# Kernel optimization log

Hardware: AMD Instinct MI355X
Metric: run time of the kernel (lower is better)

The kernel has to match this reference:

```python
import jax, jax.numpy as jnp
import numpy as np

# Uniform 3-level taxonomy: 128 roots, branching 16 then 16.
N0, B1, B2 = 128, 16, 16
N1, N2 = N0 * B1, N0 * B1 * B2          # 2048, 32768
TOTAL = N0 + N1 + N2                    # 34944
BATCH = 1024
W = (1.0, 1.0, 1.0)                     # level_weights
NEG = -100000000.0                      # fill value used by the torch module


def _ce(logits, tgt):
    # per-sample cross entropy, reduction='none': logits [B,C], tgt [B] -> [B]
    return -jnp.take_along_axis(jax.nn.log_softmax(logits, axis=-1), tgt[:, None], axis=1)[:, 0]


def setup_inputs() -> dict:
    key = jax.random.key(0)
    k1, k2, k3, k4 = jax.random.split(key, 4)
    outputs = jax.random.normal(k1, (BATCH, TOTAL), dtype=jnp.float32)
    # hierarchically consistent labels (relative-within-level ids, as labelmap expects)
    r0 = jax.random.randint(k2, (BATCH,), 0, N0, dtype=jnp.int32)
    r1 = jax.random.randint(k3, (BATCH,), 0, B1, dtype=jnp.int32)
    r2 = jax.random.randint(k4, (BATCH,), 0, B2, dtype=jnp.int32)
    lab1 = r0 * B1 + r1
    lab2 = lab1 * B2 + r2
    level_labels = jnp.stack([r0, lab1, lab2], axis=1)  # [B, 3] int32
    return {"outputs": outputs, "level_labels": level_labels}


def reference(outputs, level_labels):
    lab0, lab1, lab2 = level_labels[:, 0], level_labels[:, 1], level_labels[:, 2]
    r1 = lab1 - lab0 * B1   # new_level_labels[1]: label relative to true parent's children
    r2 = lab2 - lab1 * B2   # new_level_labels[2]

    out0 = outputs[:, :N0]                 # [B, N0]
    out1 = outputs[:, N0:N0 + N1]          # [B, N1]
    out2 = outputs[:, N0 + N1:]            # [B, N2]

    # ---- level 0: possible children == all roots, so masked CE == full CE
    loss0 = _ce(out0, lab0)
    pred0 = jnp.argmax(out0, axis=1).astype(jnp.int32)          # predicted root (relative)
    found0 = pred0 != lab0                                      # found_incorrect after level 0

    # ---- level 1
    g1_true = jnp.take_along_axis(out1.reshape(BATCH, N0, B1), lab0[:, None, None], axis=1)[:, 0, :]
    loss1 = jnp.where(found0, _ce(out1, lab1), _ce(g1_true, r1))
    g1_pred = jnp.take_along_axis(out1.reshape(BATCH, N0, B1), pred0[:, None, None], axis=1)[:, 0, :]
    pred1_in = jnp.argmax(g1_pred, axis=1).astype(jnp.int32)    # argmax within predicted parent's children
    pred1 = pred0 * B1 + pred1_in                               # predicted level-1 class (relative)
    found1 = found0 | (pred1_in != r1)

    # ---- level 2
    g2_true = jnp.take_along_axis(out2.reshape(BATCH, N1, B2), lab1[:, None, None], axis=1)[:, 0, :]
    loss2 = jnp.where(found1, _ce(out2, lab2), _ce(g2_true, r2))

    # ---- outputs_new: level-0 slice fully copied; levels 1/2 only children of the predicted path
    mask1 = (jnp.arange(N1, dtype=jnp.int32) // B1)[None, :] == pred0[:, None]
    mask2 = (jnp.arange(N2, dtype=jnp.int32) // B2)[None, :] == pred1[:, None]
    outputs_new = jnp.concatenate(
        [out0, jnp.where(mask1, out1, NEG), jnp.where(mask2, out2, NEG)], axis=1)

    # torch accumulates size-1 tensors; torch.mean of the final [1] tensor == total sum
    loss = jnp.sum(W[0] * loss0 + W[1] * loss1 + W[2] * loss2)
    return outputs_new, loss
```

## Files before the change

### kernel.cpp

```cpp
#include <hip/hip_runtime.h>
#include <math.h>

#define N0v 128
#define B1v 16
#define B2v 16
#define N1v 2048
#define N2v 32768
#define TOTALv 34944
#define BATCHv 1024
#define NEGV -100000000.0f

typedef __attribute__((ext_vector_type(4))) float f32x4;

__global__ __launch_bounds__(1024) void row_kernel(
    const float* __restrict__ outs, const int* __restrict__ labels,
    float* __restrict__ out, float* __restrict__ partials)
{
    const int b   = blockIdx.x;
    const int tid = threadIdx.x;
    const int wid = tid >> 6, lane = tid & 63;
    const float* rowp = outs + (size_t)b * TOTALv;
    float*       orow = out  + (size_t)b * TOTALv;
    const f32x4* rv4 = reinterpret_cast<const f32x4*>(rowp);
    f32x4*       ov4 = reinterpret_cast<f32x4*>(orow);
    const f32x4  neg4 = {NEGV, NEGV, NEGV, NEGV};

    __shared__ float s_wmax[2]; __shared__ int s_wmi[2];
    __shared__ float s_r[16][3];
    __shared__ float s_f[1];
    __shared__ int   s_i[2];
    __shared__ float s_g[2];

    const int lab0 = labels[b * 3 + 0];
    const int lab1 = labels[b * 3 + 1];
    const int lab2 = labels[b * 3 + 2];

    float v0 = -INFINITY;
    if (tid < N0v) v0 = rowp[tid];
    f32x4 a = {0.f, 0.f, 0.f, 0.f};
    if (tid < 512) a = rv4[32 + tid];
    const f32x4* b2 = rv4 + 544;
    f32x4*       o2 = ov4 + 544;
    const f32x4 x0 = b2[tid];
    const f32x4 x1 = b2[tid + 1024];
    const f32x4 x2 = b2[tid + 2048];
    const f32x4 x3 = b2[tid + 3072];
    const f32x4 x4 = b2[tid + 4096];
    const f32x4 x5 = b2[tid + 5120];
    const f32x4 x6 = b2[tid + 6144];
    const f32x4 x7 = b2[tid + 7168];
    __builtin_amdgcn_sched_barrier(0);

    float mv = v0; int mi = tid;
    #pragma unroll
    for (int off = 32; off; off >>= 1) {
        float ov = __shfl_down(mv, off);
        int   oi = __shfl_down(mi, off);
        if (ov > mv || (ov == mv && oi < mi)) { mv = ov; mi = oi; }
    }
    if (tid < N0v && lane == 0) { s_wmax[wid] = mv; s_wmi[wid] = mi; }
    __syncthreads();
    if (tid == 0) {
        float m0 = s_wmax[0]; int i0 = s_wmi[0];
        if (s_wmax[1] > m0 || (s_wmax[1] == m0 && s_wmi[1] < i0)) { m0 = s_wmax[1]; i0 = s_wmi[1]; }
        s_f[0] = m0; s_i[0] = i0;
    }
    __syncthreads();
    const float max0  = s_f[0];
    const int   pred0 = s_i[0];

    if (tid < 16) {
        float gp = rowp[N0v + pred0 * B1v + tid]; int gi = tid;
        #pragma unroll
        for (int off = 8; off; off >>= 1) {
            float ogp = __shfl_xor(gp, off, 16);
            int   ogi = __shfl_xor(gi, off, 16);
            if (ogp > gp || (ogp == gp && ogi < gi)) { gp = ogp; gi = ogi; }
        }
        if (tid == 0) s_i[1] = gi;
    } else if (tid < 32) {
        float eg = __expf(rowp[N0v + lab0 * B1v + (tid - 16)]);
        #pragma unroll
        for (int off = 8; off; off >>= 1) eg += __shfl_xor(eg, off, 16);
        if (tid == 16) s_g[0] = eg;
    } else if (tid < 48) {
        float eg = __expf(rowp[N0v + N1v + lab1 * B2v + (tid - 32)]);
        #pragma unroll
        for (int off = 8; off; off >>= 1) eg += __shfl_xor(eg, off, 16);
        if (tid == 32) s_g[1] = eg;
    }
    __syncthreads();
    const int pred1_in = s_i[1];
    const int pred1    = pred0 * B1v + pred1_in;

    float s1 = 0.f;
    if (tid < 512) {
        s1 = __expf(a.x) + __expf(a.y) + __expf(a.z) + __expf(a.w);
        __builtin_nontemporal_store((tid >> 2) == pred0 ? a : neg4, &ov4[32 + tid]);
        if (tid < N0v) __builtin_nontemporal_store(v0, &orow[tid]);
    }

    float s2 = 0.f;
    s2 += __expf(x0.x)+__expf(x0.y)+__expf(x0.z)+__expf(x0.w);
    __builtin_nontemporal_store(((tid       ) >> 2) == pred1 ? x0 : neg4, &o2[tid]);
    s2 += __expf(x1.x)+__expf(x1.y)+__expf(x1.z)+__expf(x1.w);
    __builtin_nontemporal_store(((tid + 1024) >> 2) == pred1 ? x1 : neg4, &o2[tid + 1024]);
    s2 += __expf(x2.x)+__expf(x2.y)+__expf(x2.z)+__expf(x2.w);
    __builtin_nontemporal_store(((tid + 2048) >> 2) == pred1 ? x2 : neg4, &o2[tid + 2048]);
    s2 += __expf(x3.x)+__expf(x3.y)+__expf(x3.z)+__expf(x3.w);
    __builtin_nontemporal_store(((tid + 3072) >> 2) == pred1 ? x3 : neg4, &o2[tid + 3072]);
    s2 += __expf(x4.x)+__expf(x4.y)+__expf(x4.z)+__expf(x4.w);
    __builtin_nontemporal_store(((tid + 4096) >> 2) == pred1 ? x4 : neg4, &o2[tid + 4096]);
    s2 += __expf(x5.x)+__expf(x5.y)+__expf(x5.z)+__expf(x5.w);
    __builtin_nontemporal_store(((tid + 5120) >> 2) == pred1 ? x5 : neg4, &o2[tid + 5120]);
    s2 += __expf(x6.x)+__expf(x6.y)+__expf(x6.z)+__expf(x6.w);
    __builtin_nontemporal_store(((tid + 6144) >> 2) == pred1 ? x6 : neg4, &o2[tid + 6144]);
    s2 += __expf(x7.x)+__expf(x7.y)+__expf(x7.z)+__expf(x7.w);
    __builtin_nontemporal_store(((tid + 7168) >> 2) == pred1 ? x7 : neg4, &o2[tid + 7168]);

    float r0 = (tid < N0v) ? __expf(v0 - max0) : 0.f;
    #pragma unroll
    for (int off = 32; off; off >>= 1) {
        r0 += __shfl_down(r0, off);
        s1 += __shfl_down(s1, off);
        s2 += __shfl_down(s2, off);
    }
    if (lane == 0) { s_r[wid][0] = r0; s_r[wid][1] = s1; s_r[wid][2] = s2; }
    __syncthreads();
    if (tid == 0) {
        float S0 = 0.f, S1 = 0.f, S2 = 0.f;
        #pragma unroll
        for (int w = 0; w < 16; ++w) { S0 += s_r[w][0]; S1 += s_r[w][1]; S2 += s_r[w][2]; }
        const float Sg1 = s_g[0], Sg2 = s_g[1];
        const int r1 = lab1 - lab0 * B1v;
        const bool found0 = (pred0 != lab0);
        const bool found1 = found0 || (pred1_in != r1);
        const float t0 = rowp[lab0];
        const float t1 = rowp[N0v + lab1];
        const float t2 = rowp[N0v + N1v + lab2];
        const float loss0 = __logf(S0) + max0 - t0;
        const float loss1 = (found0 ? __logf(S1) : __logf(Sg1)) - t1;
        const float loss2 = (found1 ? __logf(S2) : __logf(Sg2)) - t2;
        partials[b] = loss0 + loss1 + loss2;
    }
}

__global__ __launch_bounds__(256) void loss_reduce(
    const float* __restrict__ partials, float* __restrict__ out_loss)
{
    __shared__ float sh[4];
    const int tid = threadIdx.x;
    float s = 0.f;
    for (int i = tid; i < BATCHv; i += 256) s += partials[i];
    #pragma unroll
    for (int off = 32; off; off >>= 1) s += __shfl_down(s, off);
    if ((tid & 63) == 0) sh[tid >> 6] = s;
    __syncthreads();
    if (tid == 0) *out_loss = sh[0] + sh[1] + sh[2] + sh[3];
}

extern "C" void kernel_launch(void* const* d_in, const int* in_sizes, int n_in,
                              void* d_out, int out_size, void* d_ws, size_t ws_size,
                              hipStream_t stream) {
    const float* outs   = (const float*)d_in[0];
    const int*   labels = (const int*)d_in[1];
    float*       out    = (float*)d_out;
    float*       part   = (float*)d_ws;

    row_kernel<<<BATCHv, 1024, 0, stream>>>(outs, labels, out, part);
    loss_reduce<<<1, 256, 0, stream>>>(part, out + (size_t)BATCHv * TOTALv);
}
```

Before: 53.46 us.

## Split each row across two 512-thread blocks and cut per-row sync barriers

Each row is now handled by two 512-thread blocks, each taking half of the level-2 slice. The level-1 group sums and argmaxes are computed once for all 128 groups from registers, so the dependent pred0 gather and its barriers go away. Stores are deferred until after a single barrier, and the level-2 log-sum is combined across the two halves in the finalize kernel. The max subtraction for level 0 is dropped, which risks overflow with unbounded inputs, and level-1 data is loaded twice per row.

```diff
diff --git a/kernel.cpp b/kernel.cpp
--- a/kernel.cpp
+++ b/kernel.cpp
@@ -12,151 +12,157 @@
 
 typedef __attribute__((ext_vector_type(4))) float f32x4;
 
-__global__ __launch_bounds__(1024) void row_kernel(
+__global__ __launch_bounds__(512, 8) void row_kernel(
     const float* __restrict__ outs, const int* __restrict__ labels,
-    float* __restrict__ out, float* __restrict__ partials)
+    float* __restrict__ out, float* __restrict__ s2p, float* __restrict__ lb)
 {
-    const int b   = blockIdx.x;
+    const int blk = blockIdx.x;
+    const int row = blk >> 1;
+    const int j   = blk & 1;
     const int tid = threadIdx.x;
     const int wid = tid >> 6, lane = tid & 63;
-    const float* rowp = outs + (size_t)b * TOTALv;
-    float*       orow = out  + (size_t)b * TOTALv;
+    const float* rowp = outs + (size_t)row * TOTALv;
+    float*       orow = out  + (size_t)row * TOTALv;
     const f32x4* rv4 = reinterpret_cast<const f32x4*>(rowp);
     f32x4*       ov4 = reinterpret_cast<f32x4*>(orow);
     const f32x4  neg4 = {NEGV, NEGV, NEGV, NEGV};
 
+    __shared__ float sm_gsum[128];
+    __shared__ int   sm_gidx[128];
     __shared__ float s_wmax[2]; __shared__ int s_wmi[2];
-    __shared__ float s_r[16][3];
-    __shared__ float s_f[1];
+    __shared__ float s_red[8][3];
     __shared__ int   s_i[2];
-    __shared__ float s_g[2];
 
-    const int lab0 = labels[b * 3 + 0];
-    const int lab1 = labels[b * 3 + 1];
-    const int lab2 = labels[b * 3 + 2];
+    const int lab0 = labels[row * 3 + 0];
+    const int lab1 = labels[row * 3 + 1];
+    const int lab2 = labels[row * 3 + 2];
 
-    float v0 = -INFINITY;
+    float v0 = 0.f;
     if (tid < N0v) v0 = rowp[tid];
-    f32x4 a = {0.f, 0.f, 0.f, 0.f};
-    if (tid < 512) a = rv4[32 + tid];
-    const f32x4* b2 = rv4 + 544;
-    f32x4*       o2 = ov4 + 544;
-    const f32x4 x0 = b2[tid];
-    const f32x4 x1 = b2[tid + 1024];
-    const f32x4 x2 = b2[tid + 2048];
-    const f32x4 x3 = b2[tid + 3072];
-    const f32x4 x4 = b2[tid + 4096];
-    const f32x4 x5 = b2[tid + 5120];
-    const f32x4 x6 = b2[tid + 6144];
-    const f32x4 x7 = b2[tid + 7168];
+    const f32x4 a = rv4[32 + tid];
+    const f32x4* b2 = rv4 + 544 + j * 4096;
+    f32x4*       o2 = ov4 + 544 + j * 4096;
+    const f32x4 x0 = b2[tid];            const f32x4 x1 = b2[tid +  512];
+    const f32x4 x2 = b2[tid + 1024];     const f32x4 x3 = b2[tid + 1536];
+    const f32x4 x4 = b2[tid + 2048];     const f32x4 x5 = b2[tid + 2560];
+    const f32x4 x6 = b2[tid + 3072];     const f32x4 x7 = b2[tid + 3584];
+    float eg2 = 0.f;
+    if (tid < 16) eg2 = rowp[N0v + N1v + lab1 * B2v + tid];
+    float t0 = 0.f, t1 = 0.f, t2 = 0.f;
+    if (tid == 0) { t0 = rowp[lab0]; t1 = rowp[N0v + lab1]; t2 = rowp[N0v + N1v + lab2]; }
     __builtin_amdgcn_sched_barrier(0);
 
-    float mv = v0; int mi = tid;
-    #pragma unroll
-    for (int off = 32; off; off >>= 1) {
-        float ov = __shfl_down(mv, off);
-        int   oi = __shfl_down(mi, off);
-        if (ov > mv || (ov == mv && oi < mi)) { mv = ov; mi = oi; }
+    float s1 = __expf(a.x) + __expf(a.y) + __expf(a.z) + __expf(a.w);
+    float gm = a.x; int gi = 0;
+    if (a.y > gm) { gm = a.y; gi = 1; }
+    if (a.z > gm) { gm = a.z; gi = 2; }
+    if (a.w > gm) { gm = a.w; gi = 3; }
+    gi += (tid & 3) * 4;
+    float gs = s1;
+    {
+        float ov = __shfl_xor(gm, 1); int oi = __shfl_xor(gi, 1);
+        gs += __shfl_xor(gs, 1);
+        if (ov > gm || (ov == gm && oi < gi)) { gm = ov; gi = oi; }
+        ov = __shfl_xor(gm, 2); oi = __shfl_xor(gi, 2);
+        gs += __shfl_xor(gs, 2);
+        if (ov > gm || (ov == gm && oi < gi)) { gm = ov; gi = oi; }
     }
-    if (tid < N0v && lane == 0) { s_wmax[wid] = mv; s_wmi[wid] = mi; }
-    __syncthreads();
-    if (tid == 0) {
-        float m0 = s_wmax[0]; int i0 = s_wmi[0];
-        if (s_wmax[1] > m0 || (s_wmax[1] == m0 && s_wmi[1] < i0)) { m0 = s_wmax[1]; i0 = s_wmi[1]; }
-        s_f[0] = m0; s_i[0] = i0;
+    if ((tid & 3) == 0) { sm_gsum[tid >> 2] = gs; sm_gidx[tid >> 2] = gi; }
+
+    if (tid < N0v) {
+        float mv = v0; int mi = tid;
+        #pragma unroll
+        for (int off = 32; off; off >>= 1) {
+            float ov = __shfl_down(mv, off);
+            int   oi = __shfl_down(mi, off);
+            if (ov > mv || (ov == mv && oi < mi)) { mv = ov; mi = oi; }
+        }
+        if (lane == 0) { s_wmax[wid] = mv; s_wmi[wid] = mi; }
     }
-    __syncthreads();
-    const float max0  = s_f[0];
-    const int   pred0 = s_i[0];
 
     if (tid < 16) {
-        float gp = rowp[N0v + pred0 * B1v + tid]; int gi = tid;
+        eg2 = __expf(eg2);
         #pragma unroll
-        for (int off = 8; off; off >>= 1) {
-            float ogp = __shfl_xor(gp, off, 16);
-            int   ogi = __shfl_xor(gi, off, 16);
-            if (ogp > gp || (ogp == gp && ogi < gi)) { gp = ogp; gi = ogi; }
-        }
-        if (tid == 0) s_i[1] = gi;
-    } else if (tid < 32) {
-        float eg = __expf(rowp[N0v + lab0 * B1v + (tid - 16)]);
-        #pragma unroll
-        for (int off = 8; off; off >>= 1) eg += __shfl_xor(eg, off, 16);
-        if (tid == 16) s_g[0] = eg;
-    } else if (tid < 48) {
-        float eg = __expf(rowp[N0v + N1v + lab1 * B2v + (tid - 32)]);
-        #pragma unroll
-        for (int off = 8; off; off >>= 1) eg += __shfl_xor(eg, off, 16);
-        if (tid == 32) s_g[1] = eg;
-    }
-    __syncthreads();
-    const int pred1_in = s_i[1];
-    const int pred1    = pred0 * B1v + pred1_in;
-
-    float s1 = 0.f;
-    if (tid < 512) {
-        s1 = __expf(a.x) + __expf(a.y) + __expf(a.z) + __expf(a.w);
-        __builtin_nontemporal_store((tid >> 2) == pred0 ? a : neg4, &ov4[32 + tid]);
-        if (tid < N0v) __builtin_nontemporal_store(v0, &orow[tid]);
+        for (int off = 8; off; off >>= 1) eg2 += __shfl_xor(eg2, off);
     }
 
     float s2 = 0.f;
     s2 += __expf(x0.x)+__expf(x0.y)+__expf(x0.z)+__expf(x0.w);
-    __builtin_nontemporal_store(((tid       ) >> 2) == pred1 ? x0 : neg4, &o2[tid]);
     s2 += __expf(x1.x)+__expf(x1.y)+__expf(x1.z)+__expf(x1.w);
-    __builtin_nontemporal_store(((tid + 1024) >> 2) == pred1 ? x1 : neg4, &o2[tid + 1024]);
     s2 += __expf(x2.x)+__expf(x2.y)+__expf(x2.z)+__expf(x2.w);
-    __builtin_nontemporal_store(((tid + 2048) >> 2) == pred1 ? x2 : neg4, &o2[tid + 2048]);
     s2 += __expf(x3.x)+__expf(x3.y)+__expf(x3.z)+__expf(x3.w);
-    __builtin_nontemporal_store(((tid + 3072) >> 2) == pred1 ? x3 : neg4, &o2[tid + 3072]);
     s2 += __expf(x4.x)+__expf(x4.y)+__expf(x4.z)+__expf(x4.w);
-    __builtin_nontemporal_store(((tid + 4096) >> 2) == pred1 ? x4 : neg4, &o2[tid + 4096]);
     s2 += __expf(x5.x)+__expf(x5.y)+__expf(x5.z)+__expf(x5.w);
-    __builtin_nontemporal_store(((tid + 5120) >> 2) == pred1 ? x5 : neg4, &o2[tid + 5120]);
     s2 += __expf(x6.x)+__expf(x6.y)+__expf(x6.z)+__expf(x6.w);
-    __builtin_nontemporal_store(((tid + 6144) >> 2) == pred1 ? x6 : neg4, &o2[tid + 6144]);
     s2 += __expf(x7.x)+__expf(x7.y)+__expf(x7.z)+__expf(x7.w);
-    __builtin_nontemporal_store(((tid + 7168) >> 2) == pred1 ? x7 : neg4, &o2[tid + 7168]);
 
-    float r0 = (tid < N0v) ? __expf(v0 - max0) : 0.f;
+    float r0 = (tid < N0v) ? __expf(v0) : 0.f;
     #pragma unroll
     for (int off = 32; off; off >>= 1) {
         r0 += __shfl_down(r0, off);
         s1 += __shfl_down(s1, off);
         s2 += __shfl_down(s2, off);
     }
-    if (lane == 0) { s_r[wid][0] = r0; s_r[wid][1] = s1; s_r[wid][2] = s2; }
+    if (lane == 0) { s_red[wid][0] = r0; s_red[wid][1] = s1; s_red[wid][2] = s2; }
+
     __syncthreads();
+
     if (tid == 0) {
+        float m0 = s_wmax[0]; int p0 = s_wmi[0];
+        if (s_wmax[1] > m0 || (s_wmax[1] == m0 && s_wmi[1] < p0)) { m0 = s_wmax[1]; p0 = s_wmi[1]; }
+        const int p1i = sm_gidx[p0];
+        s_i[0] = p0; s_i[1] = p1i;
         float S0 = 0.f, S1 = 0.f, S2 = 0.f;
         #pragma unroll
-        for (int w = 0; w < 16; ++w) { S0 += s_r[w][0]; S1 += s_r[w][1]; S2 += s_r[w][2]; }
-        const float Sg1 = s_g[0], Sg2 = s_g[1];
-        const int r1 = lab1 - lab0 * B1v;
-        const bool found0 = (pred0 != lab0);
-        const bool found1 = found0 || (pred1_in != r1);
-        const float t0 = rowp[lab0];
-        const float t1 = rowp[N0v + lab1];
-        const float t2 = rowp[N0v + N1v + lab2];
-        const float loss0 = __logf(S0) + max0 - t0;
-        const float loss1 = (found0 ? __logf(S1) : __logf(Sg1)) - t1;
-        const float loss2 = (found1 ? __logf(S2) : __logf(Sg2)) - t2;
-        partials[b] = loss0 + loss1 + loss2;
+        for (int w = 0; w < 8; ++w) { S0 += s_red[w][0]; S1 += s_red[w][1]; S2 += s_red[w][2]; }
+        s2p[row * 2 + j] = S2;
+        if (j == 0) {
+            const float Sg1 = sm_gsum[lab0];
+            const int r1 = lab1 - lab0 * B1v;
+            const bool found0 = (p0 != lab0);
+            const bool found1 = found0 || (p1i != r1);
+            const float loss01 = (__logf(S0) - t0)
+                               + ((found0 ? __logf(S1) : __logf(Sg1)) - t1);
+            lb[row * 2 + 0] = loss01 - t2 + (found1 ? 0.f : __logf(eg2));
+            lb[row * 2 + 1] = found1 ? 1.f : 0.f;
+        }
     }
+    __syncthreads();
+    const int pred0 = s_i[0];
+    const int pred1 = pred0 * B1v + s_i[1];
+
+    if (j == 0 && tid < N0v) __builtin_nontemporal_store(v0, &orow[tid]);
+    if ((tid >> 8) == j)
+        __builtin_nontemporal_store(((tid >> 2) == pred0) ? a : neg4, &ov4[32 + tid]);
+    const int lbase = j * 4096;
+    __builtin_nontemporal_store((((lbase + tid       ) >> 2) == pred1) ? x0 : neg4, &o2[tid]);
+    __builtin_nontemporal_store((((lbase + tid +  512) >> 2) == pred1) ? x1 : neg4, &o2[tid +  512]);
+    __builtin_nontemporal_store((((lbase + tid + 1024) >> 2) == pred1) ? x2 : neg4, &o2[tid + 1024]);
+    __builtin_nontemporal_store((((lbase + tid + 1536) >> 2) == pred1) ? x3 : neg4, &o2[tid + 1536]);
+    __builtin_nontemporal_store((((lbase + tid + 2048) >> 2) == pred1) ? x4 : neg4, &o2[tid + 2048]);
+    __builtin_nontemporal_store((((lbase + tid + 2560) >> 2) == pred1) ? x5 : neg4, &o2[tid + 2560]);
+    __builtin_nontemporal_store((((lbase + tid + 3072) >> 2) == pred1) ? x6 : neg4, &o2[tid + 3072]);
+    __builtin_nontemporal_store((((lbase + tid + 3584) >> 2) == pred1) ? x7 : neg4, &o2[tid + 3584]);
 }
 
-__global__ __launch_bounds__(256) void loss_reduce(
-    const float* __restrict__ partials, float* __restrict__ out_loss)
+__global__ __launch_bounds__(1024) void finalize_kernel(
+    const float* __restrict__ s2p, const float* __restrict__ lb,
+    float* __restrict__ out_loss)
 {
-    __shared__ float sh[4];
-    const int tid = threadIdx.x;
-    float s = 0.f;
-    for (int i = tid; i < BATCHv; i += 256) s += partials[i];
+    const int r = threadIdx.x;
+    const float S2 = s2p[r * 2] + s2p[r * 2 + 1];
+    float loss = lb[r * 2] + lb[r * 2 + 1] * __logf(S2);
     #pragma unroll
-    for (int off = 32; off; off >>= 1) s += __shfl_down(s, off);
-    if ((tid & 63) == 0) sh[tid >> 6] = s;
+    for (int off = 32; off; off >>= 1) loss += __shfl_down(loss, off);
+    __shared__ float sh[16];
+    if ((r & 63) == 0) sh[r >> 6] = loss;
     __syncthreads();
-    if (tid == 0) *out_loss = sh[0] + sh[1] + sh[2] + sh[3];
+    if (r == 0) {
+        float t = 0.f;
+        #pragma unroll
+        for (int w = 0; w < 16; ++w) t += sh[w];
+        *out_loss = t;
+    }
 }
 
 extern "C" void kernel_launch(void* const* d_in, const int* in_sizes, int n_in,
@@ -165,8 +171,9 @@
     const float* outs   = (const float*)d_in[0];
     const int*   labels = (const int*)d_in[1];
     float*       out    = (float*)d_out;
-    float*       part   = (float*)d_ws;
+    float* s2p = (float*)d_ws;
+    float* lb  = (float*)d_ws + 2048;
 
-    row_kernel<<<BATCHv, 1024, 0, stream>>>(outs, labels, out, part);
-    loss_reduce<<<1, 256, 0, stream>>>(part, out + (size_t)BATCHv * TOTALv);
+    row_kernel<<<BATCHv * 2, 512, 0, stream>>>(outs, labels, out, s2p, lb);
+    finalize_kernel<<<1, 1024, 0, stream>>>(s2p, lb, out + (size_t)BATCHv * TOTALv);
 }
```

Measured after the change: 60.69 us. 13.5% more time.
